# Kernel optimization log

Hardware: AMD Instinct MI355X
Metric: run time of the kernel (lower is better)

Reference implementation:

```python
import jax, jax.numpy as jnp
import numpy as np

N = 50000
E = 800000
IN_F = 128
HID_F = 128
OUT_F = 64


def setup_inputs() -> dict:
    key = jax.random.key(0)
    ks = jax.random.split(key, 12)
    x = jax.random.normal(ks[0], (N, IN_F), dtype=jnp.float32)
    row0 = jax.random.randint(ks[1], (E,), 0, N, dtype=jnp.int32)
    col0 = jax.random.randint(ks[2], (E,), 0, N, dtype=jnp.int32)
    val0 = jax.random.uniform(ks[3], (E,), dtype=jnp.float32)
    row1 = jax.random.randint(ks[4], (E,), 0, N, dtype=jnp.int32)
    col1 = jax.random.randint(ks[5], (E,), 0, N, dtype=jnp.int32)
    val1 = jax.random.uniform(ks[6], (E,), dtype=jnp.float32)
    # GraphConvolution params, uniform(-stdv, stdv) with stdv = 1/sqrt(out_features)
    s0 = 1.0 / np.sqrt(HID_F)
    W0 = jax.random.uniform(ks[7], (IN_F, HID_F), minval=-s0, maxval=s0, dtype=jnp.float32)
    b0 = jax.random.uniform(ks[8], (HID_F,), minval=-s0, maxval=s0, dtype=jnp.float32)
    s1 = 1.0 / np.sqrt(OUT_F)
    W1 = jax.random.uniform(ks[9], (HID_F, OUT_F), minval=-s1, maxval=s1, dtype=jnp.float32)
    b1 = jax.random.uniform(ks[10], (OUT_F,), minval=-s1, maxval=s1, dtype=jnp.float32)
    return {"x": x, "row0": row0, "col0": col0, "val0": val0,
            "row1": row1, "col1": col1, "val1": val1,
            "W0": W0, "b0": b0, "W1": W1, "b1": b1}


def _gcn_layer(x, W, b, row, col, val):
    # support = x @ W ; out = spmm(adj, support) + b
    support = x @ W                       # [N, F_out]
    msgs = val[:, None] * support[col]    # [E, F_out] gather along edges
    out = jax.ops.segment_sum(msgs, row, num_segments=N)
    return out + b


def reference(x, row0, col0, val0, row1, col1, val1, W0, b0, W1, b1):
    # Layer 0: GC -> relu (dropout is identity in eval mode)
    h = _gcn_layer(x, W0, b0, row0, col0, val0)
    h = jax.nn.relu(h)
    # Layer 1 (final): GC only
    out = _gcn_layer(h, W1, b1, row1, col1, val1)
    return out
```

## Files before the change

### kernel.cpp

```cpp
#include <hip/hip_runtime.h>
#include <hip/hip_fp16.h>
#include <type_traits>

#define N_NODES 50000
#define IN_F    128
#define HID_F   128
#define OUT_F   64
#define E_EDGES 800000

#define RPB   128
#define NBUCK ((N_NODES + RPB - 1) / RPB)
#define BCAP  2560
#define BIN_T   512
#define BIN_EPT 16
#define BIN_EPB (BIN_T * BIN_EPT)
#define BIN_NB  ((E_EDGES + BIN_EPB - 1) / BIN_EPB)

typedef _Float16 half8 __attribute__((ext_vector_type(8)));
typedef float    floatx4 __attribute__((ext_vector_type(4)));

__global__ __launch_bounds__(256) void prep_kernel(const float* __restrict__ W0,
                                                   const float* __restrict__ W1,
                                                   __half* __restrict__ wt0,
                                                   __half* __restrict__ wt1,
                                                   int* __restrict__ gfill) {
    int tid = blockIdx.x * 256 + threadIdx.x;
    if (tid < IN_F * HID_F) {
        int k = tid >> 7, n = tid & 127;
        wt0[n * IN_F + k] = __float2half(W0[tid]);
    }
    if (tid < HID_F * OUT_F) {
        int k = tid / OUT_F, n = tid % OUT_F;
        wt1[n * HID_F + k] = __float2half(W1[tid]);
    }
    if (tid < 2 * NBUCK) gfill[tid] = 0;
}

template<int K, int NF, bool RELU_A, typename AT>
__global__ __launch_bounds__(256) void gemm_mfma_kernel(const AT* __restrict__ A,
                                                        const __half* __restrict__ Wt,
                                                        __half* __restrict__ C, int M) {
    constexpr int KP = K + 8;
    constexpr int NT = NF / 16;
    __shared__ _Float16 Ws[NF * KP];
    const int tid = threadIdx.x;
    constexpr int CH = NF * K / 8;
    for (int c = tid; c < CH; c += 256) {
        const int n = c / (K / 8), ko = (c % (K / 8)) * 8;
        *(half8*)&Ws[n * KP + ko] = *(const half8*)(Wt + n * K + ko);
    }
    __syncthreads();

    const int wv = tid >> 6, lane = tid & 63;
    const int quad = lane >> 4, l16 = lane & 15;
    const int rowb = blockIdx.x * 64 + wv * 16;
    const int arow = rowb + l16;

    floatx4 acc[NT] = {};
#pragma unroll
    for (int ks = 0; ks < K; ks += 32) {
        half8 af = {};
        if (arow < M) {
            if constexpr (std::is_same<AT, float>::value) {
                const float4* p = (const float4*)(A + (long)arow * K + ks + quad * 8);
                float4 u = p[0], w = p[1];
                af[0] = (_Float16)u.x; af[1] = (_Float16)u.y;
                af[2] = (_Float16)u.z; af[3] = (_Float16)u.w;
                af[4] = (_Float16)w.x; af[5] = (_Float16)w.y;
                af[6] = (_Float16)w.z; af[7] = (_Float16)w.w;
            } else {
                af = *(const half8*)(A + (long)arow * K + ks + quad * 8);
            }
        }
        if (RELU_A) {
            _Float16 z = (_Float16)0;
#pragma unroll
            for (int j = 0; j < 8; ++j) af[j] = af[j] > z ? af[j] : z;
        }
#pragma unroll
        for (int t = 0; t < NT; ++t) {
            half8 bf = *(const half8*)&Ws[(t * 16 + l16) * KP + ks + quad * 8];
            acc[t] = __builtin_amdgcn_mfma_f32_16x16x32_f16(af, bf, acc[t], 0, 0, 0);
        }
    }
#pragma unroll
    for (int t = 0; t < NT; ++t) {
        const int col = t * 16 + l16;
#pragma unroll
        for (int i = 0; i < 4; ++i) {
            const int row = rowb + quad * 4 + i;
            if (row < M) C[(long)row * NF + col] = __float2half(acc[t][i]);
        }
    }
}

__global__ __launch_bounds__(BIN_T) void bin_kernel(
        const int* __restrict__ row0, const int* __restrict__ col0, const float* __restrict__ val0,
        const int* __restrict__ row1, const int* __restrict__ col1, const float* __restrict__ val1,
        int* __restrict__ gfill, int2* __restrict__ bcv0, int2* __restrict__ bcv1) {
    const int g = blockIdx.y;
    const int*   rowi = g ? row1 : row0;
    const int*   coli = g ? col1 : col0;
    const float* vali = g ? val1 : val0;
    int*  gf  = gfill + g * NBUCK;
    int2* bcv = g ? bcv1 : bcv0;

    __shared__ int lhist[NBUCK];
    __shared__ int lbase[NBUCK];
    const int tid = threadIdx.x;
    for (int i = tid; i < NBUCK; i += BIN_T) lhist[i] = 0;
    __syncthreads();

    int rnk[BIN_EPT], bkt[BIN_EPT], cl[BIN_EPT], rw[BIN_EPT];
    float vl[BIN_EPT];
    const int e0 = blockIdx.x * BIN_EPB;
#pragma unroll
    for (int i = 0; i < BIN_EPT; ++i) {
        const int e = e0 + i * BIN_T + tid;
        bkt[i] = -1;
        if (e < E_EDGES) {
            const int r = rowi[e];
            rw[i] = r; cl[i] = coli[e]; vl[i] = vali[e];
            const int b = r / RPB;
            bkt[i] = b;
            rnk[i] = atomicAdd(&lhist[b], 1);
        }
    }
    __syncthreads();
    for (int i = tid; i < NBUCK; i += BIN_T) {
        const int c = lhist[i];
        lbase[i] = c ? atomicAdd(&gf[i], c) : 0;
    }
    __syncthreads();
#pragma unroll
    for (int i = 0; i < BIN_EPT; ++i) {
        if (bkt[i] >= 0) {
            const int pos = lbase[bkt[i]] + rnk[i];
            if (pos < BCAP)
                bcv[(long)bkt[i] * BCAP + pos] =
                    make_int2(((rw[i] & (RPB - 1)) << 16) | cl[i], __float_as_int(vl[i]));
        }
    }
}

#define SORT_T 512
#define SORT_EPT (BCAP / SORT_T)
__global__ __launch_bounds__(SORT_T) void sort_kernel(const int* __restrict__ gfill,
                                                      int2* __restrict__ bcv0,
                                                      int2* __restrict__ bcv1,
                                                      int* __restrict__ rs0,
                                                      int* __restrict__ rs1) {
    const int g = blockIdx.y;
    const int b = blockIdx.x;
    int2* buf = (g ? bcv1 : bcv0) + (long)b * BCAP;
    int*  rs  = (g ? rs1 : rs0) + b * (RPB + 1);

    __shared__ int2 sbuf[BCAP];
    __shared__ int  cur[RPB];
    __shared__ int  sc[RPB];
    __shared__ int  start[RPB + 1];

    const int tid = threadIdx.x;
    int cnt = gfill[g * NBUCK + b];
    if (cnt > BCAP) cnt = BCAP;

    int2 ed[SORT_EPT];
#pragma unroll
    for (int k = 0; k < SORT_EPT; ++k) {
        const int e = tid + k * SORT_T;
        if (e < cnt) ed[k] = buf[e];
    }

    if (tid < RPB) cur[tid] = 0;
    __syncthreads();
#pragma unroll
    for (int k = 0; k < SORT_EPT; ++k)
        if (tid + k * SORT_T < cnt) atomicAdd(&cur[ed[k].x >> 16], 1);
    __syncthreads();
    if (tid < RPB) sc[tid] = cur[tid];
    __syncthreads();
    for (int off = 1; off < RPB; off <<= 1) {
        int v = 0;
        if (tid < RPB && tid >= off) v = sc[tid - off];
        __syncthreads();
        if (tid < RPB) sc[tid] += v;
        __syncthreads();
    }
    if (tid < RPB) {
        start[tid + 1] = sc[tid];
        if (tid == 0) start[0] = 0;
        cur[tid] = (tid == 0) ? 0 : sc[tid - 1];
    }
    __syncthreads();
#pragma unroll
    for (int k = 0; k < SORT_EPT; ++k) {
        if (tid + k * SORT_T < cnt) {
            int pos = atomicAdd(&cur[ed[k].x >> 16], 1);
            sbuf[pos] = ed[k];
        }
    }
    __syncthreads();
#pragma unroll
    for (int k = 0; k < SORT_EPT; ++k) {
        const int e = tid + k * SORT_T;
        if (e < cnt) buf[e] = sbuf[e];
    }
    for (int i = tid; i <= RPB; i += SORT_T) rs[i] = start[i];
}

__global__ __launch_bounds__(256) void spmm_l0_kernel(const int* __restrict__ rs,
                                                      const int2* __restrict__ bcv,
                                                      const __half* __restrict__ sup,
                                                      const float* __restrict__ bias,
                                                      __half* __restrict__ out, int n) {
    const int wave = threadIdx.x >> 6;
    const int lane = threadIdx.x & 63;
    const int r = blockIdx.x * 4 + wave;
    if (r >= n) return;
    const int b  = r >> 7;
    const int rl = r & (RPB - 1);
    const int* rsb = rs + b * (RPB + 1);
    const int start = rsb[rl];
    const int end   = rsb[rl + 1];
    const int2* eb = bcv + (long)b * BCAP;
    const int f0 = lane * 2;
    float acc0 = bias[f0];
    float acc1 = bias[f0 + 1];

    for (int base = start; base < end; base += 64) {
        const int m = min(64, end - base);
        int2 cvl = make_int2(0, 0);
        if (lane < m) cvl = eb[base + lane];
        for (int j = 0; j < m; j += 8) {
            int   p[8];
            float v[8];
#pragma unroll
            for (int q = 0; q < 8; ++q) {
                p[q] = __shfl(cvl.x, j + q, 64);
                v[q] = __int_as_float(__shfl(cvl.y, j + q, 64));
            }
            __half2 s[8];
#pragma unroll
            for (int q = 0; q < 8; ++q)
                s[q] = *(const __half2*)(sup + (long)(p[q] & 0xFFFF) * HID_F + f0);
#pragma unroll
            for (int q = 0; q < 8; ++q) {
                float2 gq = __half22float2(s[q]);
                acc0 += v[q] * gq.x; acc1 += v[q] * gq.y;
            }
        }
    }
    *(__half2*)(out + (long)r * HID_F + f0) = __floats2half2_rn(acc0, acc1);
}

__global__ __launch_bounds__(256) void spmm_l1_kernel(const int* __restrict__ rs,
                                                      const int2* __restrict__ bcv,
                                                      const __half* __restrict__ sup,
                                                      const float* __restrict__ bias,
                                                      float* __restrict__ out, int n) {
    const int wave = threadIdx.x >> 6;
    const int lane = threadIdx.x & 63;
    const int r = blockIdx.x * 4 + wave;
    if (r >= n) return;
    const int b  = r >> 7;
    const int rl = r & (RPB - 1);
    const int* rsb = rs + b * (RPB + 1);
    const int start = rsb[rl];
    const int end   = rsb[rl + 1];
    const int2* eb = bcv + (long)b * BCAP;
    const int eh = lane >> 5;
    const int li = lane & 31;
    const int f0 = li * 2;
    float acc0 = eh ? 0.f : bias[f0];
    float acc1 = eh ? 0.f : bias[f0 + 1];

    for (int base = start; base < end; base += 64) {
        const int m = min(64, end - base);
        int2 cvl = make_int2(0, 0);
        if (lane < m) cvl = eb[base + lane];
        for (int j = 0; j < m; j += 16) {
            int   p[8];
            float v[8];
#pragma unroll
            for (int q = 0; q < 8; ++q) {
                const int src = j + 2 * q + eh;
                p[q] = __shfl(cvl.x, src, 64);
                v[q] = __int_as_float(__shfl(cvl.y, src, 64));
            }
            __half2 s[8];
#pragma unroll
            for (int q = 0; q < 8; ++q)
                s[q] = *(const __half2*)(sup + (long)(p[q] & 0xFFFF) * OUT_F + f0);
#pragma unroll
            for (int q = 0; q < 8; ++q) {
                float2 gq = __half22float2(s[q]);
                acc0 += v[q] * gq.x; acc1 += v[q] * gq.y;
            }
        }
    }
    acc0 += __shfl_xor(acc0, 32, 64);
    acc1 += __shfl_xor(acc1, 32, 64);
    if (eh == 0)
        *(float2*)(out + (long)r * OUT_F + f0) = make_float2(acc0, acc1);
}

extern "C" void kernel_launch(void* const* d_in, const int* in_sizes, int n_in,
                              void* d_out, int out_size, void* d_ws, size_t ws_size,
                              hipStream_t stream) {
    const float* x    = (const float*)d_in[0];
    const int*   row0 = (const int*)d_in[1];
    const int*   col0 = (const int*)d_in[2];
    const float* val0 = (const float*)d_in[3];
    const int*   row1 = (const int*)d_in[4];
    const int*   col1 = (const int*)d_in[5];
    const float* val1 = (const float*)d_in[6];
    const float* W0   = (const float*)d_in[7];
    const float* b0   = (const float*)d_in[8];
    const float* W1   = (const float*)d_in[9];
    const float* b1   = (const float*)d_in[10];
    float* out = (float*)d_out;

    const int M = N_NODES;

    __half* sup0 = (__half*)d_ws;
    __half* h    = sup0 + (long)N_NODES * HID_F;
    int2* bcv0   = (int2*)(h + (long)N_NODES * HID_F);
    int2* bcv1   = bcv0 + (long)NBUCK * BCAP;
    int*  rs0    = (int*)(bcv1 + (long)NBUCK * BCAP);
    int*  rs1    = rs0 + NBUCK * (RPB + 1);
    int*  gfill  = rs1 + NBUCK * (RPB + 1);
    __half* wt0  = (__half*)(gfill + 2 * NBUCK + 2);
    __half* wt1  = wt0 + IN_F * HID_F;
    __half* sup1 = sup0;

    const int SPMM_B = (N_NODES + 3) / 4;

    prep_kernel<<<(IN_F * HID_F + 255) / 256, 256, 0, stream>>>(W0, W1, wt0, wt1, gfill);
    bin_kernel<<<dim3(BIN_NB, 2), BIN_T, 0, stream>>>(row0, col0, val0, row1, col1, val1,
                                                      gfill, bcv0, bcv1);
    sort_kernel<<<dim3(NBUCK, 2), SORT_T, 0, stream>>>(gfill, bcv0, bcv1, rs0, rs1);

    gemm_mfma_kernel<IN_F, HID_F, false, float><<<(M + 63) / 64, 256, 0, stream>>>(x, wt0, sup0, M);
    spmm_l0_kernel<<<SPMM_B, 256, 0, stream>>>(rs0, bcv0, sup0, b0, h, N_NODES);

    gemm_mfma_kernel<HID_F, OUT_F, true, __half><<<(M + 63) / 64, 256, 0, stream>>>(h, wt1, sup1, M);
    spmm_l1_kernel<<<SPMM_B, 256, 0, stream>>>(rs1, bcv1, sup1, b1, out, N_NODES);
}
```

Baseline: 184.9 us.

## Merge bucket sort and layer-0 GEMM into one launch via blockIdx.y split

The per-bucket CSR sort and the x@W0 MFMA GEMM are independent, so they now run in a single grid: y=0,1 blocks sort the two edge lists and y=2 blocks compute 128 rows of the layer-0 support each, with a shared LDS union. This removes one launch and its serialization gap and lets the compute-bound GEMM overlap the memory-bound sort. The GEMM now uses 512-thread blocks with 8 waves of 16 rows, which changes its tiling and occupancy, and the LDS union sized for the sort may limit residency.

```diff
diff --git a/kernel.cpp b/kernel.cpp
--- a/kernel.cpp
+++ b/kernel.cpp
@@ -143,69 +143,119 @@
     }
 }
 
-#define SORT_T 512
-#define SORT_EPT (BCAP / SORT_T)
-__global__ __launch_bounds__(SORT_T) void sort_kernel(const int* __restrict__ gfill,
-                                                      int2* __restrict__ bcv0,
-                                                      int2* __restrict__ bcv1,
-                                                      int* __restrict__ rs0,
-                                                      int* __restrict__ rs1) {
-    const int g = blockIdx.y;
-    const int b = blockIdx.x;
-    int2* buf = (g ? bcv1 : bcv0) + (long)b * BCAP;
-    int*  rs  = (g ? rs1 : rs0) + b * (RPB + 1);
-
-    __shared__ int2 sbuf[BCAP];
-    __shared__ int  cur[RPB];
-    __shared__ int  sc[RPB];
-    __shared__ int  start[RPB + 1];
-
+#define MID_T 512
+#define SORT_EPT (BCAP / MID_T)
+union MidLds {
+    struct {
+        int2 sbuf[BCAP];
+        int  cur[RPB];
+        int  sc[RPB];
+        int  start[RPB + 1];
+    } s;
+    _Float16 ws[HID_F * (IN_F + 8)];
+};
+
+__global__ __launch_bounds__(MID_T) void mid_kernel(
+        const int* __restrict__ gfill, int2* __restrict__ bcv0, int2* __restrict__ bcv1,
+        int* __restrict__ rs0, int* __restrict__ rs1,
+        const float* __restrict__ x, const __half* __restrict__ wt0,
+        __half* __restrict__ sup0, int M) {
+    __shared__ MidLds lds;
     const int tid = threadIdx.x;
-    int cnt = gfill[g * NBUCK + b];
-    if (cnt > BCAP) cnt = BCAP;
-
-    int2 ed[SORT_EPT];
-#pragma unroll
-    for (int k = 0; k < SORT_EPT; ++k) {
-        const int e = tid + k * SORT_T;
-        if (e < cnt) ed[k] = buf[e];
-    }
-
-    if (tid < RPB) cur[tid] = 0;
-    __syncthreads();
-#pragma unroll
-    for (int k = 0; k < SORT_EPT; ++k)
-        if (tid + k * SORT_T < cnt) atomicAdd(&cur[ed[k].x >> 16], 1);
-    __syncthreads();
-    if (tid < RPB) sc[tid] = cur[tid];
-    __syncthreads();
-    for (int off = 1; off < RPB; off <<= 1) {
-        int v = 0;
-        if (tid < RPB && tid >= off) v = sc[tid - off];
-        __syncthreads();
-        if (tid < RPB) sc[tid] += v;
-        __syncthreads();
-    }
-    if (tid < RPB) {
-        start[tid + 1] = sc[tid];
-        if (tid == 0) start[0] = 0;
-        cur[tid] = (tid == 0) ? 0 : sc[tid - 1];
-    }
-    __syncthreads();
-#pragma unroll
-    for (int k = 0; k < SORT_EPT; ++k) {
-        if (tid + k * SORT_T < cnt) {
-            int pos = atomicAdd(&cur[ed[k].x >> 16], 1);
-            sbuf[pos] = ed[k];
-        }
-    }
-    __syncthreads();
-#pragma unroll
-    for (int k = 0; k < SORT_EPT; ++k) {
-        const int e = tid + k * SORT_T;
-        if (e < cnt) buf[e] = sbuf[e];
-    }
-    for (int i = tid; i <= RPB; i += SORT_T) rs[i] = start[i];
+
+    if (blockIdx.y < 2) {
+        const int g = blockIdx.y;
+        const int b = blockIdx.x;
+        int2* buf = (g ? bcv1 : bcv0) + (long)b * BCAP;
+        int*  rs  = (g ? rs1 : rs0) + b * (RPB + 1);
+
+        int cnt = gfill[g * NBUCK + b];
+        if (cnt > BCAP) cnt = BCAP;
+
+        int2 ed[SORT_EPT];
+#pragma unroll
+        for (int k = 0; k < SORT_EPT; ++k) {
+            const int e = tid + k * MID_T;
+            if (e < cnt) ed[k] = buf[e];
+        }
+
+        if (tid < RPB) lds.s.cur[tid] = 0;
+        __syncthreads();
+#pragma unroll
+        for (int k = 0; k < SORT_EPT; ++k)
+            if (tid + k * MID_T < cnt) atomicAdd(&lds.s.cur[ed[k].x >> 16], 1);
+        __syncthreads();
+        if (tid < RPB) lds.s.sc[tid] = lds.s.cur[tid];
+        __syncthreads();
+        for (int off = 1; off < RPB; off <<= 1) {
+            int v = 0;
+            if (tid < RPB && tid >= off) v = lds.s.sc[tid - off];
+            __syncthreads();
+            if (tid < RPB) lds.s.sc[tid] += v;
+            __syncthreads();
+        }
+        if (tid < RPB) {
+            lds.s.start[tid + 1] = lds.s.sc[tid];
+            if (tid == 0) lds.s.start[0] = 0;
+            lds.s.cur[tid] = (tid == 0) ? 0 : lds.s.sc[tid - 1];
+        }
+        __syncthreads();
+#pragma unroll
+        for (int k = 0; k < SORT_EPT; ++k) {
+            if (tid + k * MID_T < cnt) {
+                int pos = atomicAdd(&lds.s.cur[ed[k].x >> 16], 1);
+                lds.s.sbuf[pos] = ed[k];
+            }
+        }
+        __syncthreads();
+#pragma unroll
+        for (int k = 0; k < SORT_EPT; ++k) {
+            const int e = tid + k * MID_T;
+            if (e < cnt) buf[e] = lds.s.sbuf[e];
+        }
+        for (int i = tid; i <= RPB; i += MID_T) rs[i] = lds.s.start[i];
+    } else {
+        constexpr int KP = IN_F + 8;
+        constexpr int NT = HID_F / 16;
+        for (int c = tid; c < HID_F * (IN_F / 8); c += MID_T) {
+            const int n = c / (IN_F / 8), ko = (c % (IN_F / 8)) * 8;
+            *(half8*)&lds.ws[n * KP + ko] = *(const half8*)(wt0 + n * IN_F + ko);
+        }
+        __syncthreads();
+
+        const int wv = tid >> 6, lane = tid & 63;
+        const int quad = lane >> 4, l16 = lane & 15;
+        const int rowb = blockIdx.x * 128 + wv * 16;
+        const int arow = rowb + l16;
+
+        floatx4 acc[NT] = {};
+#pragma unroll
+        for (int ks = 0; ks < IN_F; ks += 32) {
+            half8 af = {};
+            if (arow < M) {
+                const float4* p = (const float4*)(x + (long)arow * IN_F + ks + quad * 8);
+                float4 u = p[0], w = p[1];
+                af[0] = (_Float16)u.x; af[1] = (_Float16)u.y;
+                af[2] = (_Float16)u.z; af[3] = (_Float16)u.w;
+                af[4] = (_Float16)w.x; af[5] = (_Float16)w.y;
+                af[6] = (_Float16)w.z; af[7] = (_Float16)w.w;
+            }
+#pragma unroll
+            for (int t = 0; t < NT; ++t) {
+                half8 bf = *(const half8*)&lds.ws[(t * 16 + l16) * KP + ks + quad * 8];
+                acc[t] = __builtin_amdgcn_mfma_f32_16x16x32_f16(af, bf, acc[t], 0, 0, 0);
+            }
+        }
+#pragma unroll
+        for (int t = 0; t < NT; ++t) {
+            const int col = t * 16 + l16;
+#pragma unroll
+            for (int i = 0; i < 4; ++i) {
+                const int row = rowb + quad * 4 + i;
+                if (row < M) sup0[(long)row * HID_F + col] = __float2half(acc[t][i]);
+            }
+        }
+    }
 }
 
 __global__ __launch_bounds__(256) void spmm_l0_kernel(const int* __restrict__ rs,
@@ -338,9 +388,9 @@
     prep_kernel<<<(IN_F * HID_F + 255) / 256, 256, 0, stream>>>(W0, W1, wt0, wt1, gfill);
     bin_kernel<<<dim3(BIN_NB, 2), BIN_T, 0, stream>>>(row0, col0, val0, row1, col1, val1,
                                                       gfill, bcv0, bcv1);
-    sort_kernel<<<dim3(NBUCK, 2), SORT_T, 0, stream>>>(gfill, bcv0, bcv1, rs0, rs1);
-
-    gemm_mfma_kernel<IN_F, HID_F, false, float><<<(M + 63) / 64, 256, 0, stream>>>(x, wt0, sup0, M);
+    mid_kernel<<<dim3(NBUCK, 3), MID_T, 0, stream>>>(gfill, bcv0, bcv1, rs0, rs1,
+                                                     x, wt0, sup0, M);
+
     spmm_l0_kernel<<<SPMM_B, 256, 0, stream>>>(rs0, bcv0, sup0, b0, h, N_NODES);
 
     gemm_mfma_kernel<HID_F, OUT_F, true, __half><<<(M + 63) / 64, 256, 0, stream>>>(h, wt1, sup1, M);
```

Result: no change. 182.5 us (-1.3%).
